# Kernel optimization log

Measured on AMD Instinct MI355X. Metric: run time of the kernel, lower is better.

## Reference

```python
import jax, jax.numpy as jnp
import numpy as np

B, L, D, H = 2, 2048, 1024, 16
HD = D // H

def setup_inputs() -> dict:
    key = jax.random.key(0)
    ks = jax.random.split(key, 9)
    s = 1.0 / np.sqrt(D)
    return {
        "x": jax.random.normal(ks[0], (B, L, D), jnp.float32),
        "Wq": jax.random.normal(ks[1], (D, D), jnp.float32) * s,
        "bq": jax.random.normal(ks[2], (D,), jnp.float32) * 0.02,
        "Wk": jax.random.normal(ks[3], (D, D), jnp.float32) * s,
        "bk": jax.random.normal(ks[4], (D,), jnp.float32) * 0.02,
        "Wv": jax.random.normal(ks[5], (D, D), jnp.float32) * s,
        "bv": jax.random.normal(ks[6], (D,), jnp.float32) * 0.02,
        "Wo": jax.random.normal(ks[7], (D, D), jnp.float32) * s,
        "bo": jax.random.normal(ks[8], (D,), jnp.float32) * 0.02,
    }

def reference(x, Wq, bq, Wk, bk, Wv, bv, Wo, bo):
    b, l, d = x.shape
    # projections -> [B, H, L, HD]
    def split_heads(t):
        return t.reshape(b, l, H, HD).transpose(0, 2, 1, 3)
    Q = split_heads(x @ Wq + bq)
    K = split_heads(x @ Wk + bk)
    V = split_heads(x @ Wv + bv)
    scores = jnp.einsum('bhqd,bhkd->bhqk', Q, K)  # [B,H,L,L]
    causal = jnp.tril(jnp.ones((l, l), bool))
    scores = jnp.where(causal, scores, -jnp.inf)
    attn = jax.nn.softmax(scores / np.sqrt(HD), axis=-1)
    ctx = jnp.einsum('bhqk,bhkd->bhqd', attn, V)
    ctx = ctx.transpose(0, 2, 1, 3).reshape(b, l, d)
    return ctx @ Wo + bo
```

## Files before the change

### kernel.cpp

```cpp
#include <hip/hip_runtime.h>
#include <stdint.h>

typedef unsigned short u16;
typedef __attribute__((ext_vector_type(8))) __bf16 bf16x8;
typedef __attribute__((ext_vector_type(4))) float f32x4;
typedef __attribute__((ext_vector_type(16))) float f32x16;

__device__ __forceinline__ u16 f2bf(float f) {
  union { float f; uint32_t u; } c; c.f = f;
  uint32_t u = c.u + 0x7fffu + ((c.u >> 16) & 1u);
  return (u16)(u >> 16);
}
__device__ __forceinline__ uint32_t cvtpk(float a, float b) {
  uint32_t r;
  asm("v_cvt_pk_bf16_f32 %0, %1, %2" : "=v"(r) : "v"(a), "v"(b));
  return r;
}

__device__ __forceinline__ void async16(const u16* g, u16* l) {
  __builtin_amdgcn_global_load_lds(
      (const __attribute__((address_space(1))) void*)g,
      (__attribute__((address_space(3))) void*)l, 16, 0, 0);
}

__device__ __forceinline__ f32x4 mfma16(bf16x8 a, bf16x8 b, f32x4 c) {
  return __builtin_amdgcn_mfma_f32_16x16x32_bf16(a, b, c, 0, 0, 0);
}
__device__ __forceinline__ f32x16 mfma32(bf16x8 a, bf16x8 b, f32x16 c) {
  return __builtin_amdgcn_mfma_f32_32x32x16_bf16(a, b, c, 0, 0, 0);
}


__global__ __launch_bounds__(256) void x_cvt_kernel(const float* __restrict__ x,
                                                    u16* __restrict__ xb) {
  int i = (blockIdx.x * 256 + threadIdx.x) * 4;
  float4 v = *(const float4*)(x + i);
  uint2 t; t.x = cvtpk(v.x, v.y); t.y = cvtpk(v.z, v.w);
  *(uint2*)(xb + i) = t;
}

__global__ __launch_bounds__(256) void wt_cvt_kernel(const float* __restrict__ Wq,
                                                     const float* __restrict__ Wk,
                                                     const float* __restrict__ Wv,
                                                     const float* __restrict__ Wo,
                                                     u16* __restrict__ out) {
  __shared__ __align__(16) u16 t[64][72];
  int z = blockIdx.z;
  const float* W = (z == 0) ? Wq : (z == 1) ? Wk : (z == 2) ? Wv : Wo;
  u16* o = out + (size_t)z * (1u << 20);
  int n0 = blockIdx.x * 64, k0 = blockIdx.y * 64;
  int tid = threadIdx.x;
  int c4 = (tid & 15) * 4, r0 = tid >> 4;
#pragma unroll
  for (int i = 0; i < 4; i++) {
    int r = r0 + i * 16;
    float4 v = *(const float4*)(W + (size_t)(k0 + r) * 1024 + n0 + c4);
    t[c4 + 0][r] = f2bf(v.x);
    t[c4 + 1][r] = f2bf(v.y);
    t[c4 + 2][r] = f2bf(v.z);
    t[c4 + 3][r] = f2bf(v.w);
  }
  __syncthreads();
  int n = tid >> 2, kc = (tid & 3) * 16;
  uint4 a = *(const uint4*)&t[n][kc];
  uint4 b = *(const uint4*)&t[n][kc + 8];
  *(uint4*)(o + (size_t)(n0 + n) * 1024 + k0 + kc) = a;
  *(uint4*)(o + (size_t)(n0 + n) * 1024 + k0 + kc + 8) = b;
}

template <int TN>
__device__ __forceinline__ void gemm_core2(const u16* __restrict__ A,
                                           const u16* __restrict__ Bt,
                                           u16* As, u16* Bs,
                                           f32x4 (&acc)[4][TN / 32]) {
  constexpr int NJ = TN / 32;
  constexpr int ASZ = 128 * 32, BSZ = TN * 32;
  const int tid = threadIdx.x, wave = tid >> 6, lane = tid & 63;
  const int low = lane & 15, hi = lane >> 4;
  const int wm = wave >> 1, wn = wave & 1;
  const int m0 = blockIdx.y * 128, n0 = blockIdx.x * TN;
  const f32x4 fzero = {0.f, 0.f, 0.f, 0.f};
#pragma unroll
  for (int i = 0; i < 4; i++)
#pragma unroll
    for (int j = 0; j < NJ; j++) acc[i][j] = fzero;

  const int ea0 = wave * 128 + lane, ea1 = ea0 + 64;
  const u16* ga0 = A + (size_t)(m0 + (ea0 >> 2)) * 1024 + (ea0 & 3) * 8;
  const u16* ga1 = A + (size_t)(m0 + (ea1 >> 2)) * 1024 + (ea1 & 3) * 8;
  u16* la0 = As + (wave * 2 + 0) * 512;
  u16* la1 = As + (wave * 2 + 1) * 512;

  const int eb0 = (TN == 128) ? (wave * 128 + lane) : (wave * 64 + lane);
  const int eb1 = eb0 + 64;
  const u16* gb0 = Bt + (size_t)(n0 + (eb0 >> 2)) * 1024 + (eb0 & 3) * 8;
  const u16* gb1 = Bt + (size_t)(n0 + (eb1 >> 2)) * 1024 + (eb1 & 3) * 8;
  u16* lb0 = Bs + ((TN == 128) ? (wave * 2 + 0) * 512 : wave * 512);
  u16* lb1 = Bs + (wave * 2 + 1) * 512;

  const u16* ap = As + (wm * 64 + low) * 32 + hi * 8;
  const u16* bp = Bs + (wn * (TN / 2) + low) * 32 + hi * 8;

#define GSTAGE(buf, KT)                                                        \
  {                                                                            \
    async16(ga0 + (KT), la0 + (buf) * ASZ);                                    \
    async16(ga1 + (KT), la1 + (buf) * ASZ);                                    \
    async16(gb0 + (KT), lb0 + (buf) * BSZ);                                    \
    if (TN == 128) async16(gb1 + (KT), lb1 + (buf) * BSZ);                     \
  }

  GSTAGE(0, 0)
  GSTAGE(1, 32)
  int buf = 0;
  for (int kt = 0; kt < 1024; kt += 32) {
    if (kt + 32 < 1024) {
      if constexpr (TN == 128) asm volatile("s_waitcnt vmcnt(4)" ::: "memory");
      else                     asm volatile("s_waitcnt vmcnt(3)" ::: "memory");
    } else {
      asm volatile("s_waitcnt vmcnt(0)" ::: "memory");
    }
    __builtin_amdgcn_s_barrier();

    bf16x8 af[4], bfv[NJ];
#pragma unroll
    for (int i = 0; i < 4; i++)
      af[i] = *(const bf16x8*)(ap + buf * ASZ + i * 16 * 32);
#pragma unroll
    for (int j = 0; j < NJ; j++)
      bfv[j] = *(const bf16x8*)(bp + buf * BSZ + j * 16 * 32);
#pragma unroll
    for (int i = 0; i < 4; i++)
#pragma unroll
      for (int j = 0; j < NJ; j++) acc[i][j] = mfma16(af[i], bfv[j], acc[i][j]);

    __builtin_amdgcn_s_barrier();
    if (kt + 64 < 1024) GSTAGE(buf, kt + 64)
    buf ^= 1;
  }
#undef GSTAGE
}

__global__ __launch_bounds__(256) void gemm_qkv_kernel(
    const u16* __restrict__ xb, const u16* __restrict__ wT,
    const float* __restrict__ bq, const float* __restrict__ bk,
    const float* __restrict__ bv,
    u16* __restrict__ qs, u16* __restrict__ ks, u16* __restrict__ vts) {
  __shared__ __align__(16) u16 smem[17440];
  u16* As = smem;
  u16* Bs = smem + 8192;
  const int z = blockIdx.z;
  const u16* Bt = wT + (size_t)z * (1u << 20);
  f32x4 acc[4][4];
  gemm_core2<128>(xb, Bt, As, Bs, acc);

  const float* bias = (z == 0) ? bq : (z == 1) ? bk : bv;
  u16* out = (z == 0) ? qs : (z == 1) ? ks : vts;
  const float scale = (z == 0) ? 0.180336880f : 1.0f;
  const int tid = threadIdx.x, wave = tid >> 6, lane = tid & 63;
  const int low = lane & 15, hi = lane >> 4;
  const int wm = wave >> 1, wn = wave & 1;
  const int m0 = blockIdx.y * 128, n0 = blockIdx.x * 128;

  const int h = (n0 >> 6) + wn;
  const int gmb = m0 + wm * 64;
  const int b = gmb >> 11;
  const int lb = gmb & 2047;

  u16* tile = smem + wave * 4360;
#pragma unroll
  for (int i = 0; i < 4; i++)
#pragma unroll
    for (int j = 0; j < 4; j++) {
      int hd = j * 16 + low;
      float bval = bias[h * 64 + hd];
#pragma unroll
      for (int r = 0; r < 4; r++) {
        int row = i * 16 + hi * 4 + r;
        tile[row * 68 + hd] = f2bf((acc[i][j][r] + bval) * scale);
      }
    }

  if (z != 2) {
    u16* dst = out + ((size_t)((b * 16 + h) * 2048 + lb + lane)) * 64;
    const u16* src = tile + lane * 68;
#pragma unroll
    for (int c = 0; c < 4; c++) {
      uint2 a0 = *(const uint2*)(src + c * 16 + 0);
      uint2 a1 = *(const uint2*)(src + c * 16 + 4);
      uint2 a2 = *(const uint2*)(src + c * 16 + 8);
      uint2 a3 = *(const uint2*)(src + c * 16 + 12);
      uint4 w0; w0.x = a0.x; w0.y = a0.y; w0.z = a1.x; w0.w = a1.y;
      uint4 w1; w1.x = a2.x; w1.y = a2.y; w1.z = a3.x; w1.w = a3.y;
      *(uint4*)(dst + c * 16 + 0) = w0;
      *(uint4*)(dst + c * 16 + 8) = w1;
    }
  } else {
    int l4 = (lane & 15) * 4;
    int lp4 = (l4 & ~12) | ((l4 & 4) << 1) | ((l4 & 8) >> 1);
    int ghd = lane >> 4;
    u16* vbase = out + ((size_t)(b * 16 + h) * 64) * 2048 + lb + lp4;
#pragma unroll
    for (int s = 0; s < 16; s++) {
      int hd = s * 4 + ghd;
      uint32_t v0 = tile[(l4 + 0) * 68 + hd];
      uint32_t v1 = tile[(l4 + 1) * 68 + hd];
      uint32_t v2 = tile[(l4 + 2) * 68 + hd];
      uint32_t v3 = tile[(l4 + 3) * 68 + hd];
      uint2 w; w.x = v0 | (v1 << 16); w.y = v2 | (v3 << 16);
      *(uint2*)(vbase + (size_t)hd * 2048) = w;
    }
  }
}

__global__ __launch_bounds__(256) void gemm_out_kernel(
    const u16* __restrict__ ctx, const u16* __restrict__ woT,
    const float* __restrict__ bo, float* __restrict__ out) {
  __shared__ __align__(16) u16 As[2 * 128 * 32];
  __shared__ __align__(16) u16 Bs[2 * 64 * 32];
  f32x4 acc[4][2];
  gemm_core2<64>(ctx, woT, As, Bs, acc);
  const int tid = threadIdx.x, wave = tid >> 6, lane = tid & 63;
  const int low = lane & 15, hi = lane >> 4;
  const int wm = wave >> 1, wn = wave & 1;
  const int m0 = blockIdx.y * 128, n0 = blockIdx.x * 64;
#pragma unroll
  for (int i = 0; i < 4; i++)
#pragma unroll
    for (int j = 0; j < 2; j++) {
      int gn = n0 + wn * 32 + j * 16 + low;
      float bval = bo[gn];
#pragma unroll
      for (int r = 0; r < 4; r++) {
        int gm = m0 + wm * 64 + i * 16 + hi * 4 + r;
        out[(size_t)gm * 1024 + gn] = acc[i][j][r] + bval;
      }
    }
}

__global__ __launch_bounds__(512) void flash_kernel(
    const u16* __restrict__ Qs, const u16* __restrict__ Ks,
    const u16* __restrict__ Vts, u16* __restrict__ ctx) {
  __shared__ __align__(16) u16 Kls[2][2][64 * 64];
  __shared__ __align__(16) u16 Vls[2][2][64 * 64];

  const int bid = blockIdx.x;
  const int qt = (bid < 256) ? (15 - (bid >> 5)) : ((bid - 256) >> 5);
  const int bh = bid & 31;
  const int qb = qt * 128;
  const int nT = qt + 1;

  const int tid = threadIdx.x, wave = tid >> 6, lane = tid & 63;
  const int wq = wave & 3, g = wave >> 2;
  const int q32 = lane & 31, hi2 = lane >> 5;
  const int x7 = q32 & 7;

  const u16* Qb = Qs + (size_t)bh * (2048 * 64);
  const u16* Kb = Ks + (size_t)bh * (2048 * 64);
  const u16* Vb = Vts + (size_t)bh * (64 * 2048);

  const int qrow = qb + wq * 32 + q32;
  bf16x8 qf[4];
#pragma unroll
  for (int ds = 0; ds < 4; ds++)
    qf[ds] = *(const bf16x8*)(Qb + (size_t)qrow * 64 + ds * 16 + hi2 * 8);

  f32x16 o0, o1;
#pragma unroll
  for (int r = 0; r < 16; r++) { o0[r] = 0.f; o1[r] = 0.f; }
  float m_ = -1e30f, l_ = 0.f;

#define STAGE(buf, KT0)                                                        \
  {                                                                            \
    _Pragma("unroll") for (int i = 0; i < 2; i++) {                            \
      int row = (wq * 2 + i) * 8 + (lane >> 3);                                \
      async16(Kb + (size_t)((KT0) + row) * 64 +                                \
                  (((lane & 7) ^ (row & 7)) * 8),                              \
              &Kls[g][buf][(wq * 2 + i) * 512]);                               \
      async16(Vb + (size_t)row * 2048 + (KT0) +                                \
                  (((lane & 7) ^ (row & 7)) * 8),                              \
              &Vls[g][buf][(wq * 2 + i) * 512]);                               \
    }                                                                          \
  }

  const int tb = g * nT;
  STAGE(0, (tb + 0) * 64)
  STAGE(1, (tb + 1) * 64)

  const int qmax = qb + wq * 32 + 31;

  int cur = 0;
  for (int t = 0; t < nT; t++) {
    const int kt0 = (tb + t) * 64;
    if (t + 1 < nT) { asm volatile("s_waitcnt vmcnt(4)" ::: "memory"); }
    else            { asm volatile("s_waitcnt vmcnt(0)" ::: "memory"); }
    __builtin_amdgcn_s_barrier();

    if (kt0 <= qmax) {
      const u16* Kc = &Kls[g][cur][0];
      const u16* Vc = &Vls[g][cur][0];

      f32x16 s0, s1;
#pragma unroll
      for (int r = 0; r < 16; r++) { s0[r] = 0.f; s1[r] = 0.f; }
      __builtin_amdgcn_s_setprio(1);
#pragma unroll
      for (int ds = 0; ds < 4; ds++) {
        int cs = ((ds * 2 + hi2) ^ x7) * 8;
        bf16x8 kf0 = *(const bf16x8*)(Kc + q32 * 64 + cs);
        bf16x8 kf1 = *(const bf16x8*)(Kc + (32 + q32) * 64 + cs);
        s0 = mfma32(kf0, qf[ds], s0);
        s1 = mfma32(kf1, qf[ds], s1);
      }
      __builtin_amdgcn_s_setprio(0);

      bf16x8 vf0[4], vf1[4];
#pragma unroll
      for (int ksx = 0; ksx < 4; ksx++) {
        int sc = ((2 * ksx + hi2) ^ x7) * 8;
        vf0[ksx] = *(const bf16x8*)(Vc + q32 * 64 + sc);
        vf1[ksx] = *(const bf16x8*)(Vc + (32 + q32) * 64 + sc);
      }

      if (kt0 + 63 > qb + wq * 32) {
#pragma unroll
        for (int r = 0; r < 16; r++) {
          int kl = (r & 3) + 8 * (r >> 2) + 4 * hi2;
          if (kt0 + kl > qrow) s0[r] = -1e30f;
          if (kt0 + 32 + kl > qrow) s1[r] = -1e30f;
        }
      }

      float pm = -1e30f;
#pragma unroll
      for (int r = 0; r < 16; r++) pm = fmaxf(pm, fmaxf(s0[r], s1[r]));
      pm = fmaxf(pm, __shfl_xor(pm, 32));
      if (__any(pm > m_ + 8.f)) {
        float mn = fmaxf(m_, pm);
        float corr = __builtin_amdgcn_exp2f(m_ - mn);
        m_ = mn;
        l_ *= corr;
#pragma unroll
        for (int r = 0; r < 16; r++) { o0[r] *= corr; o1[r] *= corr; }
      }

      float rs = 0.f;
#pragma unroll
      for (int r = 0; r < 16; r++) {
        s0[r] = __builtin_amdgcn_exp2f(s0[r] - m_);
        s1[r] = __builtin_amdgcn_exp2f(s1[r] - m_);
        rs += s0[r] + s1[r];
      }
      rs += __shfl_xor(rs, 32);
      l_ += rs;

      bf16x8 pb[4];
#pragma unroll
      for (int ksx = 0; ksx < 4; ksx++) {
        union { uint32_t u[4]; bf16x8 v; } pu;
        if (ksx < 2) {
          int rb = 8 * ksx;
          pu.u[0] = cvtpk(s0[rb + 0], s0[rb + 1]);
          pu.u[1] = cvtpk(s0[rb + 2], s0[rb + 3]);
          pu.u[2] = cvtpk(s0[rb + 4], s0[rb + 5]);
          pu.u[3] = cvtpk(s0[rb + 6], s0[rb + 7]);
        } else {
          int rb = 8 * (ksx - 2);
          pu.u[0] = cvtpk(s1[rb + 0], s1[rb + 1]);
          pu.u[1] = cvtpk(s1[rb + 2], s1[rb + 3]);
          pu.u[2] = cvtpk(s1[rb + 4], s1[rb + 5]);
          pu.u[3] = cvtpk(s1[rb + 6], s1[rb + 7]);
        }
        pb[ksx] = pu.v;
      }

      __builtin_amdgcn_s_setprio(1);
#pragma unroll
      for (int ksx = 0; ksx < 4; ksx++) {
        o0 = mfma32(vf0[ksx], pb[ksx], o0);
        o1 = mfma32(vf1[ksx], pb[ksx], o1);
      }
      __builtin_amdgcn_s_setprio(0);
    }

    __builtin_amdgcn_s_barrier();
    if (t + 2 < nT) STAGE(cur, (tb + t + 2) * 64)
    cur ^= 1;
  }

  __syncthreads();
  float* mb = (float*)&Kls[0][0][0] + wq * 2304;
  if (g == 1) {
#pragma unroll
    for (int m = 0; m < 4; m++) {
      f32x4 qa = {o0[4 * m + 0], o0[4 * m + 1], o0[4 * m + 2], o0[4 * m + 3]};
      f32x4 qb2 = {o1[4 * m + 0], o1[4 * m + 1], o1[4 * m + 2], o1[4 * m + 3]};
      *(f32x4*)(mb + m * 256 + (lane << 2)) = qa;
      *(f32x4*)(mb + (4 + m) * 256 + (lane << 2)) = qb2;
    }
    mb[2048 + (lane << 1) + 0] = m_;
    mb[2048 + (lane << 1) + 1] = l_;
  }
  __syncthreads();
  if (g == 0) {
    float m1 = mb[2048 + (lane << 1) + 0];
    float l1 = mb[2048 + (lane << 1) + 1];
    float mm = fmaxf(m_, m1);
    float cA = __builtin_amdgcn_exp2f(m_ - mm);
    float cB = __builtin_amdgcn_exp2f(m1 - mm);
    l_ = l_ * cA + l1 * cB;
#pragma unroll
    for (int m = 0; m < 4; m++) {
      f32x4 qa = *(const f32x4*)(mb + m * 256 + (lane << 2));
      f32x4 qb2 = *(const f32x4*)(mb + (4 + m) * 256 + (lane << 2));
#pragma unroll
      for (int j = 0; j < 4; j++) {
        o0[4 * m + j] = o0[4 * m + j] * cA + qa[j] * cB;
        o1[4 * m + j] = o1[4 * m + j] * cA + qb2[j] * cB;
      }
    }

    const int b = bh >> 4, h = bh & 15;
    float inv = 1.f / l_;
    size_t base = ((size_t)(b * 2048 + qrow)) * 1024 + h * 64;
#pragma unroll
    for (int m = 0; m < 4; m++) {
      uint2 w0, w1;
      w0.x = cvtpk(o0[4 * m + 0] * inv, o0[4 * m + 1] * inv);
      w0.y = cvtpk(o0[4 * m + 2] * inv, o0[4 * m + 3] * inv);
      *(uint2*)(ctx + base + 8 * m + 4 * hi2) = w0;
      w1.x = cvtpk(o1[4 * m + 0] * inv, o1[4 * m + 1] * inv);
      w1.y = cvtpk(o1[4 * m + 2] * inv, o1[4 * m + 3] * inv);
      *(uint2*)(ctx + base + 32 + 8 * m + 4 * hi2) = w1;
    }
  }
}


extern "C" void kernel_launch(void* const* d_in, const int* in_sizes, int n_in,
                              void* d_out, int out_size, void* d_ws, size_t ws_size,
                              hipStream_t stream) {
  const float* x  = (const float*)d_in[0];
  const float* Wq = (const float*)d_in[1];
  const float* bq = (const float*)d_in[2];
  const float* Wk = (const float*)d_in[3];
  const float* bk = (const float*)d_in[4];
  const float* Wv = (const float*)d_in[5];
  const float* bv = (const float*)d_in[6];
  const float* Wo = (const float*)d_in[7];
  const float* bo = (const float*)d_in[8];

  char* ws = (char*)d_ws;
  u16* xb  = (u16*)(ws);
  u16* wT  = (u16*)(ws + (8u << 20));
  u16* qs  = (u16*)(ws + (16u << 20));
  u16* ks  = (u16*)(ws + (24u << 20));
  u16* vts = (u16*)(ws + (32u << 20));
  u16* ctx = (u16*)(ws + (40u << 20));

  x_cvt_kernel<<<4096, 256, 0, stream>>>(x, xb);
  wt_cvt_kernel<<<dim3(16, 16, 4), 256, 0, stream>>>(Wq, Wk, Wv, Wo, wT);
  gemm_qkv_kernel<<<dim3(8, 32, 3), 256, 0, stream>>>(xb, wT, bq, bk, bv, qs, ks, vts);
  flash_kernel<<<512, 512, 0, stream>>>(qs, ks, vts, ctx);
  gemm_out_kernel<<<dim3(16, 32), 256, 0, stream>>>(ctx, wT + 3 * (1u << 20), bo, (float*)d_out);
}
```

Before: 121.4 us.

## Triple-buffer GEMM loads and remap blocks for XCD-local L2 reuse

The shared GEMM core now uses a three-stage LDS ring with deeper prefetch (kt+96) and matching vmcnt waits, so more global-to-LDS loads are in flight during MFMA work. Both GEMM kernels switch to a 1D grid with a block-index remap that gives each group of blocks (bid mod 8, presumably one per XCD) a contiguous patch of output tiles, aiming to improve L2 reuse of A and B tiles. The costs are more LDS per block, which may lower occupancy, and the remap assumes round-robin dispatch of blocks to eight XCDs.

```diff
diff --git a/kernel.cpp b/kernel.cpp
--- a/kernel.cpp
+++ b/kernel.cpp
@@ -69,16 +69,16 @@
 }
 
 template <int TN>
-__device__ __forceinline__ void gemm_core2(const u16* __restrict__ A,
+__device__ __forceinline__ void gemm_core3(const u16* __restrict__ A,
                                            const u16* __restrict__ Bt,
                                            u16* As, u16* Bs,
-                                           f32x4 (&acc)[4][TN / 32]) {
+                                           f32x4 (&acc)[4][TN / 32],
+                                           int m0, int n0) {
   constexpr int NJ = TN / 32;
   constexpr int ASZ = 128 * 32, BSZ = TN * 32;
   const int tid = threadIdx.x, wave = tid >> 6, lane = tid & 63;
   const int low = lane & 15, hi = lane >> 4;
   const int wm = wave >> 1, wn = wave & 1;
-  const int m0 = blockIdx.y * 128, n0 = blockIdx.x * TN;
   const f32x4 fzero = {0.f, 0.f, 0.f, 0.f};
 #pragma unroll
   for (int i = 0; i < 4; i++)
@@ -111,9 +111,13 @@
 
   GSTAGE(0, 0)
   GSTAGE(1, 32)
+  GSTAGE(2, 64)
   int buf = 0;
   for (int kt = 0; kt < 1024; kt += 32) {
-    if (kt + 32 < 1024) {
+    if (kt + 96 <= 1024) {
+      if constexpr (TN == 128) asm volatile("s_waitcnt vmcnt(8)" ::: "memory");
+      else                     asm volatile("s_waitcnt vmcnt(6)" ::: "memory");
+    } else if (kt + 64 <= 1024) {
       if constexpr (TN == 128) asm volatile("s_waitcnt vmcnt(4)" ::: "memory");
       else                     asm volatile("s_waitcnt vmcnt(3)" ::: "memory");
     } else {
@@ -134,8 +138,8 @@
       for (int j = 0; j < NJ; j++) acc[i][j] = mfma16(af[i], bfv[j], acc[i][j]);
 
     __builtin_amdgcn_s_barrier();
-    if (kt + 64 < 1024) GSTAGE(buf, kt + 64)
-    buf ^= 1;
+    if (kt + 96 < 1024) GSTAGE(buf, kt + 96)
+    buf = (buf == 2) ? 0 : buf + 1;
   }
 #undef GSTAGE
 }
@@ -145,13 +149,22 @@
     const float* __restrict__ bq, const float* __restrict__ bk,
     const float* __restrict__ bv,
     u16* __restrict__ qs, u16* __restrict__ ks, u16* __restrict__ vts) {
-  __shared__ __align__(16) u16 smem[17440];
+  __shared__ __align__(16) u16 smem[24576];
   u16* As = smem;
-  u16* Bs = smem + 8192;
-  const int z = blockIdx.z;
+  u16* Bs = smem + 12288;
+
+  const int bid = blockIdx.x;
+  const int c = bid & 7;
+  const int j = bid >> 3;
+  const int z = j >> 5;
+  const int jj = j & 31;
+  const int ytile = (c >> 1) * 8 + (jj >> 2);
+  const int xtile = (c & 1) * 4 + (jj & 3);
+  const int m0 = ytile * 128, n0 = xtile * 128;
+
   const u16* Bt = wT + (size_t)z * (1u << 20);
   f32x4 acc[4][4];
-  gemm_core2<128>(xb, Bt, As, Bs, acc);
+  gemm_core3<128>(xb, Bt, As, Bs, acc, m0, n0);
 
   const float* bias = (z == 0) ? bq : (z == 1) ? bk : bv;
   u16* out = (z == 0) ? qs : (z == 1) ? ks : vts;
@@ -159,7 +172,6 @@
   const int tid = threadIdx.x, wave = tid >> 6, lane = tid & 63;
   const int low = lane & 15, hi = lane >> 4;
   const int wm = wave >> 1, wn = wave & 1;
-  const int m0 = blockIdx.y * 128, n0 = blockIdx.x * 128;
 
   const int h = (n0 >> 6) + wn;
   const int gmb = m0 + wm * 64;
@@ -170,13 +182,13 @@
 #pragma unroll
   for (int i = 0; i < 4; i++)
 #pragma unroll
-    for (int j = 0; j < 4; j++) {
-      int hd = j * 16 + low;
+    for (int jx = 0; jx < 4; jx++) {
+      int hd = jx * 16 + low;
       float bval = bias[h * 64 + hd];
 #pragma unroll
       for (int r = 0; r < 4; r++) {
         int row = i * 16 + hi * 4 + r;
-        tile[row * 68 + hd] = f2bf((acc[i][j][r] + bval) * scale);
+        tile[row * 68 + hd] = f2bf((acc[i][jx][r] + bval) * scale);
       }
     }
 
@@ -184,15 +196,15 @@
     u16* dst = out + ((size_t)((b * 16 + h) * 2048 + lb + lane)) * 64;
     const u16* src = tile + lane * 68;
 #pragma unroll
-    for (int c = 0; c < 4; c++) {
-      uint2 a0 = *(const uint2*)(src + c * 16 + 0);
-      uint2 a1 = *(const uint2*)(src + c * 16 + 4);
-      uint2 a2 = *(const uint2*)(src + c * 16 + 8);
-      uint2 a3 = *(const uint2*)(src + c * 16 + 12);
+    for (int cc = 0; cc < 4; cc++) {
+      uint2 a0 = *(const uint2*)(src + cc * 16 + 0);
+      uint2 a1 = *(const uint2*)(src + cc * 16 + 4);
+      uint2 a2 = *(const uint2*)(src + cc * 16 + 8);
+      uint2 a3 = *(const uint2*)(src + cc * 16 + 12);
       uint4 w0; w0.x = a0.x; w0.y = a0.y; w0.z = a1.x; w0.w = a1.y;
       uint4 w1; w1.x = a2.x; w1.y = a2.y; w1.z = a3.x; w1.w = a3.y;
-      *(uint4*)(dst + c * 16 + 0) = w0;
-      *(uint4*)(dst + c * 16 + 8) = w1;
+      *(uint4*)(dst + cc * 16 + 0) = w0;
+      *(uint4*)(dst + cc * 16 + 8) = w1;
     }
   } else {
     int l4 = (lane & 15) * 4;
@@ -215,24 +227,31 @@
 __global__ __launch_bounds__(256) void gemm_out_kernel(
     const u16* __restrict__ ctx, const u16* __restrict__ woT,
     const float* __restrict__ bo, float* __restrict__ out) {
-  __shared__ __align__(16) u16 As[2 * 128 * 32];
-  __shared__ __align__(16) u16 Bs[2 * 64 * 32];
+  __shared__ __align__(16) u16 As[3 * 128 * 32];
+  __shared__ __align__(16) u16 Bs[3 * 64 * 32];
+
+  const int bid = blockIdx.x;
+  const int c = bid & 7;
+  const int j = bid >> 3;
+  const int ytile = (c >> 1) * 8 + (j >> 3);
+  const int xtile = (c & 1) * 8 + (j & 7);
+  const int m0 = ytile * 128, n0 = xtile * 64;
+
   f32x4 acc[4][2];
-  gemm_core2<64>(ctx, woT, As, Bs, acc);
+  gemm_core3<64>(ctx, woT, As, Bs, acc, m0, n0);
   const int tid = threadIdx.x, wave = tid >> 6, lane = tid & 63;
   const int low = lane & 15, hi = lane >> 4;
   const int wm = wave >> 1, wn = wave & 1;
-  const int m0 = blockIdx.y * 128, n0 = blockIdx.x * 64;
 #pragma unroll
   for (int i = 0; i < 4; i++)
 #pragma unroll
-    for (int j = 0; j < 2; j++) {
-      int gn = n0 + wn * 32 + j * 16 + low;
+    for (int jx = 0; jx < 2; jx++) {
+      int gn = n0 + wn * 32 + jx * 16 + low;
       float bval = bo[gn];
 #pragma unroll
       for (int r = 0; r < 4; r++) {
         int gm = m0 + wm * 64 + i * 16 + hi * 4 + r;
-        out[(size_t)gm * 1024 + gn] = acc[i][j][r] + bval;
+        out[(size_t)gm * 1024 + gn] = acc[i][jx][r] + bval;
       }
     }
 }
@@ -413,9 +432,9 @@
       f32x4 qa = *(const f32x4*)(mb + m * 256 + (lane << 2));
       f32x4 qb2 = *(const f32x4*)(mb + (4 + m) * 256 + (lane << 2));
 #pragma unroll
-      for (int j = 0; j < 4; j++) {
-        o0[4 * m + j] = o0[4 * m + j] * cA + qa[j] * cB;
-        o1[4 * m + j] = o1[4 * m + j] * cA + qb2[j] * cB;
+      for (int jx = 0; jx < 4; jx++) {
+        o0[4 * m + jx] = o0[4 * m + jx] * cA + qa[jx] * cB;
+        o1[4 * m + jx] = o1[4 * m + jx] * cA + qb2[jx] * cB;
       }
     }
 
@@ -459,7 +478,7 @@
 
   x_cvt_kernel<<<4096, 256, 0, stream>>>(x, xb);
   wt_cvt_kernel<<<dim3(16, 16, 4), 256, 0, stream>>>(Wq, Wk, Wv, Wo, wT);
-  gemm_qkv_kernel<<<dim3(8, 32, 3), 256, 0, stream>>>(xb, wT, bq, bk, bv, qs, ks, vts);
+  gemm_qkv_kernel<<<768, 256, 0, stream>>>(xb, wT, bq, bk, bv, qs, ks, vts);
   flash_kernel<<<512, 512, 0, stream>>>(qs, ks, vts, ctx);
-  gemm_out_kernel<<<dim3(16, 32), 256, 0, stream>>>(ctx, wT + 3 * (1u << 20), bo, (float*)d_out);
-}
+  gemm_out_kernel<<<512, 256, 0, stream>>>(ctx, wT + 3 * (1u << 20), bo, (float*)d_out);
+}
```

New measurement: 114.5 us. -5.6%, faster.
